# Kernel tuning notes

Hardware: AMD Instinct MI355X
Metric: run time of the kernel (lower is better)

## Reference

```python
import jax, jax.numpy as jnp
import numpy as np

B, L, D = 8, 8192, 512   # batch, seq_len (q_len == kv_len), model dim
H, K = 8, 64             # heads, head_dim
W = 128                  # chunk width == stride (non-overlapping chunks)


def setup_inputs() -> dict:
    key = jax.random.key(0)
    ks = jax.random.split(key, 6)
    s = 1.0 / np.sqrt(D)
    return {
        "inputs_q": jax.random.normal(ks[0], (B, L, D), jnp.float32),
        "inputs_kv": jax.random.normal(ks[1], (B, L, D), jnp.float32),
        "Wq": jax.random.normal(ks[2], (D, H, K), jnp.float32) * s,
        "Wk": jax.random.normal(ks[3], (D, H, K), jnp.float32) * s,
        "Wv": jax.random.normal(ks[4], (D, H, K), jnp.float32) * s,
        "Wo": jax.random.normal(ks[5], (H, K, D), jnp.float32) * s,
    }


def reference(inputs_q, inputs_kv, Wq, Wk, Wv, Wo):
    # LocalAttentionLayer with q/kv_chunk_width == stride == W and
    # always_attend_to_first_position=True. Since width == stride the chunks
    # are non-overlapping, so the per-chunk Python loop of the original is
    # equivalent to a batched reshape into [B, C, W, ...] chunks. QKV
    # projections are position-wise, so projecting the full sequence first is
    # exactly the same math as projecting each chunk.
    C = L // W  # number of chunks
    scale = 1.0 / jnp.sqrt(jnp.asarray(K, inputs_q.dtype))

    q = jnp.einsum('bld,dhk->blhk', inputs_q, Wq) * scale  # [B,L,H,K]
    k = jnp.einsum('bld,dhk->blhk', inputs_kv, Wk)
    v = jnp.einsum('bld,dhk->blhk', inputs_kv, Wv)

    qc = q.reshape(B, C, W, H, K)
    kc = k.reshape(B, C, W, H, K)
    vc = v.reshape(B, C, W, H, K)

    # Global first KV position ([CLS]) prepended to every chunk's keys/values,
    # matching `kv_cls = inputs_kv[..., 0:1, :]; concat([kv_cls, chunk])`.
    k_cls = jnp.broadcast_to(k[:, None, 0:1], (B, C, 1, H, K))
    v_cls = jnp.broadcast_to(v[:, None, 0:1], (B, C, 1, H, K))
    kc = jnp.concatenate([k_cls, kc], axis=2)  # [B,C,W+1,H,K]
    vc = jnp.concatenate([v_cls, vc], axis=2)

    scores = jnp.einsum('bcqhk,bcmhk->bchqm', qc, kc)  # [B,C,H,W,W+1]
    attn = jax.nn.softmax(scores, axis=-1)
    ctx = jnp.einsum('bchqm,bcmhk->bcqhk', attn, vc)   # [B,C,W,H,K]
    ctx = ctx.reshape(B, L, H, K)
    return jnp.einsum('blhk,hkd->bld', ctx, Wo)        # [B,L,D]
```

## Files before the change

kernel.cpp:

```cpp
#include <hip/hip_runtime.h>
#include <hip/hip_bf16.h>
#include <type_traits>

#define B_ 8
#define L_ 8192
#define D_ 512
#define H_ 8
#define KD_ 64
#define W_ 128
#define C_ 64
#define M_ (B_ * L_)
#define HK_ 512

typedef __bf16 bf16_t;
typedef __bf16 bf16x8 __attribute__((ext_vector_type(8)));
typedef float f32x4 __attribute__((ext_vector_type(4)));

#define GLOAD16(gp, lp)                                                        \
  __builtin_amdgcn_global_load_lds(                                            \
      (const __attribute__((address_space(1))) unsigned int*)(gp),             \
      (__attribute__((address_space(3))) unsigned int*)(lp), 16, 0, 0)

#define WAIT_LGKM0()                                                           \
  do {                                                                         \
    asm volatile("s_waitcnt lgkmcnt(0)" ::: "memory");                         \
    __builtin_amdgcn_sched_barrier(0);                                         \
  } while (0)

#define MFMA16(AF, BF, ACC, OFF)                                               \
  do {                                                                         \
    __builtin_amdgcn_s_setprio(1);                                             \
    _Pragma("unroll") for (int i_ = 0; i_ < 4; i_++)                           \
        _Pragma("unroll") for (int j_ = 0; j_ < 4; j_++)                       \
            ACC[i_ + OFF][j_] = __builtin_amdgcn_mfma_f32_16x16x32_bf16(       \
                AF[i_], BF[j_], ACC[i_ + OFF][j_], 0, 0, 0);                   \
    __builtin_amdgcn_s_setprio(0);                                             \
  } while (0)

__global__ void prep_weights_kernel(const float* __restrict__ Wq,
                                    const float* __restrict__ Wk,
                                    const float* __restrict__ Wv,
                                    const float* __restrict__ Wo,
                                    bf16_t* __restrict__ wt) {
  __shared__ float t[64][65];
  const int tid = threadIdx.x;
  const int mat = blockIdx.z;
  const float* src = (mat == 0) ? Wq : (mat == 1) ? Wk : (mat == 2) ? Wv : Wo;
  const float scale = (mat == 0) ? 0.125f : 1.0f;
  const int d0 = blockIdx.x * 64, n0 = blockIdx.y * 64;
  const int c = tid & 63, rb = tid >> 6;
#pragma unroll
  for (int i = 0; i < 16; i++) {
    const int r = i * 4 + rb;
    t[r][c] = src[(size_t)(d0 + r) * 512 + n0 + c];
  }
  __syncthreads();
#pragma unroll
  for (int i = 0; i < 16; i++) {
    const int n = i * 4 + rb;
    wt[((size_t)mat * 512 + n0 + n) * 512 + d0 + c] = (bf16_t)(t[c][n] * scale);
  }
}

__device__ __forceinline__ bf16x8 rdfrag(const bf16_t* region, int rowbase,
                                         int lane) {
  const int fr = lane & 15;
  const int fs = (lane >> 4) ^ ((lane >> 1) & 3);
  return *reinterpret_cast<const bf16x8*>(region + (rowbase + fr) * 32 + fs * 8);
}

__device__ __forceinline__ void rdA_raw(const float* region, int rowbase,
                                        int lane, f32x4* o) {
  const int fr = lane & 15;
  const int g = lane >> 4;
  const int row = rowbase + fr;
  const int sw = (row >> 1) & 3;
  const float* sub = region + (g >> 1) * 4096;
  const int s0 = (g & 1) << 1;
  o[0] = *reinterpret_cast<const f32x4*>(sub + row * 16 + ((s0 | 0) ^ sw) * 4);
  o[1] = *reinterpret_cast<const f32x4*>(sub + row * 16 + ((s0 | 1) ^ sw) * 4);
}

__device__ __forceinline__ bf16x8 cvtA(const f32x4* r) {
  bf16x8 o;
  o[0] = (bf16_t)r[0][0]; o[1] = (bf16_t)r[0][1];
  o[2] = (bf16_t)r[0][2]; o[3] = (bf16_t)r[0][3];
  o[4] = (bf16_t)r[1][0]; o[5] = (bf16_t)r[1][1];
  o[6] = (bf16_t)r[1][2]; o[7] = (bf16_t)r[1][3];
  return o;
}

template <int NTILE>
__global__ __launch_bounds__(512, 2)
void gemm_qkv(const float* __restrict__ A0f, const float* __restrict__ A1f,
              const bf16_t* __restrict__ BT,
              bf16_t* __restrict__ C0, bf16_t* __restrict__ C1,
              bf16_t* __restrict__ C2) {
  __shared__ __align__(16) bf16_t lds[65536];

  constexpr int NB = NTILE * 256;
  const int bid = blockIdx.x;
  const int swz = (bid & 7) * (NB / 8) + (bid >> 3);
  const int my = swz / NTILE;
  const int mx = swz - my * NTILE;
  const int m0 = my * 256;
  const int seg = mx >> 1;
  const int ncol0 = (mx & 1) * 256;
  const int nB0 = mx * 256;

  const float* const A = (seg == 0) ? A0f : A1f;
  bf16_t* const outp = (seg == 0) ? C0 : (seg == 1) ? C1 : C2;

  const int tid = threadIdx.x;
  const int lane = tid & 63;
  const int wid = tid >> 6;
  const int wmB = (wid >> 2) * 128;
  const int wnB = (wid & 3) * 64;

  const float* const Agb =
      A + ((size_t)m0 + (tid >> 2)) * 512 + (((tid & 3) ^ ((tid >> 3) & 3))) * 4;
  const int sr0 = tid >> 2;
  const int sgs = (tid & 3) ^ ((sr0 >> 1) & 3);
  const bf16_t* const Bgb = BT + ((size_t)nB0 + sr0) * 512 + sgs * 8;

  auto astage = [&](int tile, int i) {
    const int sub = i >> 1, half = i & 1;
    char* lp = (char*)lds + (tile % 3) * 32768 + sub * 16384 + half * 8192 +
               wid * 1024;
    const float* g = Agb + (size_t)half * 128 * 512 + tile * 32 + sub * 16;
    GLOAD16(g, lp);
  };
  auto bstage = [&](int tile) {
    char* lp = (char*)lds + 98304 + (tile & 1) * 16384 + wid * 1024;
    const bf16_t* g = Bgb + tile * 32;
    GLOAD16(g, lp);
    GLOAD16(g + (size_t)128 * 512, lp + 8192);
  };

  f32x4 acc[8][4] = {};
  bf16x8 b[4];

  astage(0, 0); astage(0, 1); astage(0, 2); astage(0, 3); bstage(0);
  astage(1, 0); astage(1, 1); astage(1, 2); astage(1, 3); bstage(1);
  asm volatile("s_waitcnt vmcnt(6)" ::: "memory");
  __builtin_amdgcn_s_barrier();

  for (int t = 0; t < 16; ++t) {
    const float* AR = (const float*)((char*)lds + (t % 3) * 32768);
    const bf16_t* BR = (const bf16_t*)((char*)lds + 98304 + (t & 1) * 16384);

    f32x4 ar0[4][2];
#pragma unroll
    for (int q = 0; q < 4; q++) rdA_raw(AR, wmB + q * 16, lane, ar0[q]);
#pragma unroll
    for (int q = 0; q < 4; q++) b[q] = rdfrag(BR, wnB + q * 16, lane);
    if (t < 14) { astage(t + 2, 0); astage(t + 2, 1); }
    __builtin_amdgcn_s_barrier();
    WAIT_LGKM0();
    {
      bf16x8 al[4];
#pragma unroll
      for (int q = 0; q < 4; q++) al[q] = cvtA(ar0[q]);
      MFMA16(al, b, acc, 0);
    }
    __builtin_amdgcn_s_barrier();

    f32x4 ar1[4][2];
#pragma unroll
    for (int q = 0; q < 4; q++) rdA_raw(AR, wmB + 64 + q * 16, lane, ar1[q]);
    if (t < 14) { astage(t + 2, 2); astage(t + 2, 3); bstage(t + 2); }
    __builtin_amdgcn_s_barrier();
    WAIT_LGKM0();
    {
      bf16x8 ah[4];
#pragma unroll
      for (int q = 0; q < 4; q++) ah[q] = cvtA(ar1[q]);
      MFMA16(ah, b, acc, 4);
    }
    if (t < 14) {
      asm volatile("s_waitcnt vmcnt(6)" ::: "memory");
    } else {
      asm volatile("s_waitcnt vmcnt(0)" ::: "memory");
    }
    __builtin_amdgcn_s_barrier();
  }

  const int crow = (lane >> 4) * 4;
  const int ccol = lane & 15;
#pragma unroll
  for (int i = 0; i < 8; i++) {
#pragma unroll
    for (int j = 0; j < 4; j++) {
      const int gm = m0 + wmB + i * 16 + crow;
      const int gn = ncol0 + wnB + j * 16 + ccol;
#pragma unroll
      for (int jj = 0; jj < 4; jj++)
        outp[(size_t)(gm + jj) * 512 + gn] = (bf16_t)acc[i][j][jj];
    }
  }
}

template <typename OT, int NTILE>
__global__ __launch_bounds__(512, 2)
void gemm256(const bf16_t* __restrict__ A0, const bf16_t* __restrict__ BT,
             OT* __restrict__ C0) {
  __shared__ __align__(16) bf16_t lds[65536];

  constexpr int NB = NTILE * 256;
  const int bid = blockIdx.x;
  const int swz = (bid & 7) * (NB / 8) + (bid >> 3);
  const int my = swz / NTILE;
  const int mx = swz - my * NTILE;
  const int m0 = my * 256;
  const int ncol0 = (mx & 1) * 256;
  const int nB0 = mx * 256;

  const int tid = threadIdx.x;
  const int lane = tid & 63;
  const int wid = tid >> 6;
  const int wmB = (wid >> 2) * 128;
  const int wnB = (wid & 3) * 64;

  const int sr0 = tid >> 2;
  const int sgs = (tid & 3) ^ ((sr0 >> 1) & 3);
  const bf16_t* const Agb = A0 + ((size_t)m0 + sr0) * 512 + sgs * 8;
  const bf16_t* const Bgb = BT + ((size_t)nB0 + sr0) * 512 + sgs * 8;

  auto stage = [&](int tile, int mat, int kh) {
    if (tile >= 8) return;
    bf16_t* reg = lds + ((tile & 1) * 4 + mat * 2 + kh) * 8192;
    const bf16_t* g0 = (mat == 0 ? Agb : Bgb) + tile * 64 + kh * 32;
    char* lp = (char*)reg + wid * 1024;
    GLOAD16(g0, lp);
    GLOAD16(g0 + (size_t)128 * 512, lp + 8192);
  };

  f32x4 acc[8][4] = {};
  bf16x8 a0[4], a1[4], a2[4], a3[4], b0[4], b2[4];

  stage(0, 0, 0); stage(0, 1, 0); stage(0, 0, 1); stage(0, 1, 1);
  stage(1, 1, 0); stage(1, 0, 0); stage(1, 1, 1);
  asm volatile("s_waitcnt vmcnt(6)" ::: "memory");
  __builtin_amdgcn_s_barrier();

  for (int t = 0; t < 8; ++t) {
    const int p = t & 1;
    const bf16_t* Ap0 = lds + (p * 4 + 0) * 8192;
    const bf16_t* Ap1 = lds + (p * 4 + 1) * 8192;
    const bf16_t* Bp0 = lds + (p * 4 + 2) * 8192;
    const bf16_t* Bp1 = lds + (p * 4 + 3) * 8192;

#pragma unroll
    for (int q = 0; q < 4; q++) a0[q] = rdfrag(Ap0, wmB + q * 16, lane);
#pragma unroll
    for (int q = 0; q < 4; q++) b0[q] = rdfrag(Bp0, wnB + q * 16, lane);
    stage(t + 1, 0, 1);
    __builtin_amdgcn_s_barrier();
    WAIT_LGKM0();
    if (t > 0) MFMA16(a3, b2, acc, 4);
    __builtin_amdgcn_s_barrier();

#pragma unroll
    for (int q = 0; q < 4; q++) a1[q] = rdfrag(Ap0, wmB + 64 + q * 16, lane);
    stage(t + 2, 1, 0);
    __builtin_amdgcn_s_barrier();
    WAIT_LGKM0();
    MFMA16(a0, b0, acc, 0);
    __builtin_amdgcn_s_barrier();

#pragma unroll
    for (int q = 0; q < 4; q++) a2[q] = rdfrag(Ap1, wmB + q * 16, lane);
#pragma unroll
    for (int q = 0; q < 4; q++) b2[q] = rdfrag(Bp1, wnB + q * 16, lane);
    stage(t + 2, 0, 0);
    __builtin_amdgcn_s_barrier();
    WAIT_LGKM0();
    MFMA16(a1, b0, acc, 4);
    __builtin_amdgcn_s_barrier();

#pragma unroll
    for (int q = 0; q < 4; q++) a3[q] = rdfrag(Ap1, wmB + 64 + q * 16, lane);
    stage(t + 2, 1, 1);
    __builtin_amdgcn_s_barrier();
    WAIT_LGKM0();
    MFMA16(a2, b2, acc, 0);
    if (t < 6) {
      asm volatile("s_waitcnt vmcnt(6)" ::: "memory");
    } else {
      asm volatile("s_waitcnt vmcnt(0)" ::: "memory");
    }
    __builtin_amdgcn_s_barrier();
  }

  MFMA16(a3, b2, acc, 4);

  const int crow = (lane >> 4) * 4;
  const int ccol = lane & 15;
#pragma unroll
  for (int i = 0; i < 8; i++) {
#pragma unroll
    for (int j = 0; j < 4; j++) {
      const int gm = m0 + wmB + i * 16 + crow;
      const int gn = ncol0 + wnB + j * 16 + ccol;
#pragma unroll
      for (int jj = 0; jj < 4; jj++) {
        const float vv = acc[i][j][jj];
        if constexpr (std::is_same<OT, float>::value)
          C0[(size_t)(gm + jj) * 512 + gn] = vv;
        else
          C0[(size_t)(gm + jj) * 512 + gn] = (bf16_t)vv;
      }
    }
  }
}

__global__ __launch_bounds__(256, 3)
void attn_kernel(const bf16_t* __restrict__ q, const bf16_t* __restrict__ k,
                 const bf16_t* __restrict__ v, bf16_t* __restrict__ ctx) {
  const int bid = blockIdx.x;
  const int swz = (bid & 7) * 512 + (bid >> 3);
  const int h = swz & 7;
  const int cb = swz >> 3;
  const int c = cb & 63;
  const int b = cb >> 6;

  const int tid = threadIdx.x;
  const int lane = tid & 63;
  const int w = tid >> 6;
  const int cl = lane & 15;
  const int g = lane >> 4;

  __shared__ bf16_t vT[64][136];
  __shared__ bf16_t pL[128][136];
  __shared__ float scl[128];
  __shared__ bf16_t kcls[64];
  __shared__ bf16_t vcls[64];

  const size_t headoff = (size_t)h * KD_;
  const size_t rowbase = (size_t)b * L_ + (size_t)c * W_;

  if (tid < 64) {
    kcls[tid] = k[(size_t)b * L_ * HK_ + headoff + tid];
    vcls[tid] = v[(size_t)b * L_ * HK_ + headoff + tid];
  }
  {
    const int m = tid >> 1;
    const int kd0 = (tid & 1) * 32;
    const bf16_t* vp = v + (rowbase + m) * HK_ + headoff + kd0;
#pragma unroll
    for (int i = 0; i < 4; i++) {
      bf16x8 t8 = *reinterpret_cast<const bf16x8*>(vp + i * 8);
#pragma unroll
      for (int j = 0; j < 8; j++) vT[kd0 + i * 8 + j][m] = t8[j];
    }
  }

  bf16x8 qf[2][2];
#pragma unroll
  for (int rt = 0; rt < 2; rt++)
#pragma unroll
    for (int kk = 0; kk < 2; kk++) {
      const size_t row = rowbase + w * 32 + rt * 16 + cl;
      qf[rt][kk] = *reinterpret_cast<const bf16x8*>(&q[row * HK_ + headoff + kk * 32 + g * 8]);
    }

  f32x4 sacc[2][8] = {};
#pragma unroll
  for (int ct = 0; ct < 8; ct++) {
    bf16x8 kf[2];
#pragma unroll
    for (int kk = 0; kk < 2; kk++) {
      const size_t rowm = rowbase + ct * 16 + cl;
      kf[kk] = *reinterpret_cast<const bf16x8*>(&k[rowm * HK_ + headoff + kk * 32 + g * 8]);
    }
#pragma unroll
    for (int rt = 0; rt < 2; rt++)
#pragma unroll
      for (int kk = 0; kk < 2; kk++)
        sacc[rt][ct] = __builtin_amdgcn_mfma_f32_16x16x32_bf16(qf[rt][kk], kf[kk], sacc[rt][ct], 0, 0, 0);
  }

  __syncthreads();

#pragma unroll
  for (int rt = 0; rt < 2; rt++) {
    float part = 0.f;
#pragma unroll
    for (int kk = 0; kk < 2; kk++)
#pragma unroll
      for (int j = 0; j < 8; j++)
        part += (float)qf[rt][kk][j] * (float)kcls[kk * 32 + g * 8 + j];
    part += __shfl_xor(part, 16);
    part += __shfl_xor(part, 32);
    if (g == 0) scl[w * 32 + rt * 16 + cl] = part;
  }

  float invd[2][4];
#pragma unroll
  for (int rt = 0; rt < 2; rt++) {
#pragma unroll
    for (int jj = 0; jj < 4; jj++) {
      float mx = sacc[rt][0][jj];
#pragma unroll
      for (int ct = 1; ct < 8; ct++) mx = fmaxf(mx, sacc[rt][ct][jj]);
#pragma unroll
      for (int d = 1; d < 16; d <<= 1) mx = fmaxf(mx, __shfl_xor(mx, d));
      const float sc = scl[w * 32 + rt * 16 + g * 4 + jj];
      mx = fmaxf(mx, sc);
      float sum = 0.f;
#pragma unroll
      for (int ct = 0; ct < 8; ct++) {
        const float e = __expf(sacc[rt][ct][jj] - mx);
        sacc[rt][ct][jj] = e;
        sum += e;
      }
#pragma unroll
      for (int d = 1; d < 16; d <<= 1) sum += __shfl_xor(sum, d);
      const float pc = __expf(sc - mx);
      sum += pc;
      const float inv = 1.0f / sum;
      invd[rt][jj] = inv;
      if (cl == 0) scl[w * 32 + rt * 16 + g * 4 + jj] = pc * inv;
    }
  }

#pragma unroll
  for (int rt = 0; rt < 2; rt++)
#pragma unroll
    for (int jj = 0; jj < 4; jj++) {
      const int row = w * 32 + rt * 16 + g * 4 + jj;
#pragma unroll
      for (int ct = 0; ct < 8; ct++)
        pL[row][ct * 16 + cl] = (bf16_t)(sacc[rt][ct][jj] * invd[rt][jj]);
    }
  __syncthreads();

  f32x4 cacc[2][4] = {};
#pragma unroll
  for (int kk = 0; kk < 4; kk++) {
    bf16x8 vf[4];
#pragma unroll
    for (int c2 = 0; c2 < 4; c2++)
      vf[c2] = *reinterpret_cast<const bf16x8*>(&vT[c2 * 16 + cl][kk * 32 + g * 8]);
#pragma unroll
    for (int rt = 0; rt < 2; rt++) {
      const bf16x8 pf = *reinterpret_cast<const bf16x8*>(&pL[w * 32 + rt * 16 + cl][kk * 32 + g * 8]);
#pragma unroll
      for (int c2 = 0; c2 < 4; c2++)
        cacc[rt][c2] = __builtin_amdgcn_mfma_f32_16x16x32_bf16(pf, vf[c2], cacc[rt][c2], 0, 0, 0);
    }
  }

#pragma unroll
  for (int rt = 0; rt < 2; rt++)
#pragma unroll
    for (int c2 = 0; c2 < 4; c2++)
#pragma unroll
      for (int jj = 0; jj < 4; jj++) {
        const int row = w * 32 + rt * 16 + g * 4 + jj;
        const int kd = c2 * 16 + cl;
        const float val = cacc[rt][c2][jj] + scl[row] * (float)vcls[kd];
        ctx[(rowbase + row) * HK_ + headoff + kd] = (bf16_t)val;
      }
}

extern "C" void kernel_launch(void* const* d_in, const int* in_sizes, int n_in,
                              void* d_out, int out_size, void* d_ws, size_t ws_size,
                              hipStream_t stream) {
  const float* Xq = (const float*)d_in[0];
  const float* Xkv = (const float*)d_in[1];
  const float* Wq = (const float*)d_in[2];
  const float* Wk = (const float*)d_in[3];
  const float* Wv = (const float*)d_in[4];
  const float* Wo = (const float*)d_in[5];
  float* out = (float*)d_out;

  char* ws = (char*)d_ws;
  bf16_t* wT = (bf16_t*)ws;
  size_t off = (size_t)4 * 512 * 512 * sizeof(bf16_t);
  bf16_t* qb = (bf16_t*)(ws + off); off += (size_t)M_ * HK_ * 2;
  bf16_t* kb = (bf16_t*)(ws + off); off += (size_t)M_ * HK_ * 2;
  bf16_t* vb = (bf16_t*)(ws + off); off += (size_t)M_ * HK_ * 2;
  bf16_t* ctxb = (bf16_t*)(ws + off);

  bf16_t* wTqkv = wT;
  bf16_t* wTo = wT + (size_t)3 * 512 * 512;

  prep_weights_kernel<<<dim3(8, 8, 4), 256, 0, stream>>>(Wq, Wk, Wv, Wo, wT);

  gemm_qkv<6><<<dim3(6 * (M_ / 256)), 512, 0, stream>>>(
      Xq, Xkv, wTqkv, qb, kb, vb);

  attn_kernel<<<dim3(H_ * C_ * B_), 256, 0, stream>>>(qb, kb, vb, ctxb);

  gemm256<float, 2><<<dim3(2 * (M_ / 256)), 512, 0, stream>>>(ctxb, wTo, out);
}
```

Baseline: 356.8 us.

## Write V pre-transposed per chunk/head from QKV GEMM, drop LDS transpose in attention

The QKV projection epilogue now stores V in a per-(batch, chunk, head) transposed layout [kd][row] using packed 4-element bf16 stores. The attention kernel reads V fragments directly from global memory instead of staging a transpose through LDS, which frees the vT shared array. It raises the occupancy hint from 3 to 4 blocks per SM. In exchange, V B-operand loads in the PV matmul now come from global/L2 rather than LDS, and the V stores in the GEMM epilogue are strided.

```diff
diff --git a/kernel.cpp b/kernel.cpp
--- a/kernel.cpp
+++ b/kernel.cpp
@@ -14,6 +14,7 @@
 
 typedef __bf16 bf16_t;
 typedef __bf16 bf16x8 __attribute__((ext_vector_type(8)));
+typedef __bf16 bf16x4 __attribute__((ext_vector_type(4)));
 typedef float f32x4 __attribute__((ext_vector_type(4)));
 
 #define GLOAD16(gp, lp)                                                        \
@@ -109,7 +110,6 @@
   const int nB0 = mx * 256;
 
   const float* const A = (seg == 0) ? A0f : A1f;
-  bf16_t* const outp = (seg == 0) ? C0 : (seg == 1) ? C1 : C2;
 
   const int tid = threadIdx.x;
   const int lane = tid & 63;
@@ -187,15 +187,34 @@
 
   const int crow = (lane >> 4) * 4;
   const int ccol = lane & 15;
-#pragma unroll
-  for (int i = 0; i < 8; i++) {
-#pragma unroll
-    for (int j = 0; j < 4; j++) {
-      const int gm = m0 + wmB + i * 16 + crow;
-      const int gn = ncol0 + wnB + j * 16 + ccol;
-#pragma unroll
-      for (int jj = 0; jj < 4; jj++)
-        outp[(size_t)(gm + jj) * 512 + gn] = (bf16_t)acc[i][j][jj];
+  if (seg == 2) {
+    const int cb2 = (m0 + wmB) >> 7;
+#pragma unroll
+    for (int i = 0; i < 8; i++) {
+#pragma unroll
+      for (int j = 0; j < 4; j++) {
+        const int gn = ncol0 + wnB + j * 16 + ccol;
+        const int h2 = gn >> 6, kd = gn & 63;
+        const int row = i * 16 + crow;
+        bf16x4 pk;
+#pragma unroll
+        for (int jj = 0; jj < 4; jj++) pk[jj] = (bf16_t)acc[i][j][jj];
+        *reinterpret_cast<bf16x4*>(C2 + ((size_t)(cb2 * 8 + h2)) * 8192 +
+                                   (size_t)kd * 128 + row) = pk;
+      }
+    }
+  } else {
+    bf16_t* const outp = (seg == 0) ? C0 : C1;
+#pragma unroll
+    for (int i = 0; i < 8; i++) {
+#pragma unroll
+      for (int j = 0; j < 4; j++) {
+        const int gm = m0 + wmB + i * 16 + crow;
+        const int gn = ncol0 + wnB + j * 16 + ccol;
+#pragma unroll
+        for (int jj = 0; jj < 4; jj++)
+          outp[(size_t)(gm + jj) * 512 + gn] = (bf16_t)acc[i][j][jj];
+      }
     }
   }
 }
@@ -314,9 +333,9 @@
   }
 }
 
-__global__ __launch_bounds__(256, 3)
+__global__ __launch_bounds__(256, 4)
 void attn_kernel(const bf16_t* __restrict__ q, const bf16_t* __restrict__ k,
-                 const bf16_t* __restrict__ v, bf16_t* __restrict__ ctx) {
+                 const bf16_t* __restrict__ vt, bf16_t* __restrict__ ctx) {
   const int bid = blockIdx.x;
   const int swz = (bid & 7) * 512 + (bid >> 3);
   const int h = swz & 7;
@@ -330,7 +349,6 @@
   const int cl = lane & 15;
   const int g = lane >> 4;
 
-  __shared__ bf16_t vT[64][136];
   __shared__ bf16_t pL[128][136];
   __shared__ float scl[128];
   __shared__ bf16_t kcls[64];
@@ -338,21 +356,11 @@
 
   const size_t headoff = (size_t)h * KD_;
   const size_t rowbase = (size_t)b * L_ + (size_t)c * W_;
+  const bf16_t* const vtc = vt + ((size_t)((b * 64 + c) * 8 + h)) * 8192;
 
   if (tid < 64) {
     kcls[tid] = k[(size_t)b * L_ * HK_ + headoff + tid];
-    vcls[tid] = v[(size_t)b * L_ * HK_ + headoff + tid];
-  }
-  {
-    const int m = tid >> 1;
-    const int kd0 = (tid & 1) * 32;
-    const bf16_t* vp = v + (rowbase + m) * HK_ + headoff + kd0;
-#pragma unroll
-    for (int i = 0; i < 4; i++) {
-      bf16x8 t8 = *reinterpret_cast<const bf16x8*>(vp + i * 8);
-#pragma unroll
-      for (int j = 0; j < 8; j++) vT[kd0 + i * 8 + j][m] = t8[j];
-    }
+    vcls[tid] = vt[((size_t)(b * 64 * 8 + h)) * 8192 + (size_t)tid * 128];
   }
 
   bf16x8 qf[2][2];
@@ -441,7 +449,8 @@
     bf16x8 vf[4];
 #pragma unroll
     for (int c2 = 0; c2 < 4; c2++)
-      vf[c2] = *reinterpret_cast<const bf16x8*>(&vT[c2 * 16 + cl][kk * 32 + g * 8]);
+      vf[c2] = *reinterpret_cast<const bf16x8*>(
+          &vtc[(size_t)(c2 * 16 + cl) * 128 + kk * 32 + g * 8]);
 #pragma unroll
     for (int rt = 0; rt < 2; rt++) {
       const bf16x8 pf = *reinterpret_cast<const bf16x8*>(&pL[w * 32 + rt * 16 + cl][kk * 32 + g * 8]);
@@ -480,7 +489,7 @@
   size_t off = (size_t)4 * 512 * 512 * sizeof(bf16_t);
   bf16_t* qb = (bf16_t*)(ws + off); off += (size_t)M_ * HK_ * 2;
   bf16_t* kb = (bf16_t*)(ws + off); off += (size_t)M_ * HK_ * 2;
-  bf16_t* vb = (bf16_t*)(ws + off); off += (size_t)M_ * HK_ * 2;
+  bf16_t* vtb = (bf16_t*)(ws + off); off += (size_t)M_ * HK_ * 2;
   bf16_t* ctxb = (bf16_t*)(ws + off);
 
   bf16_t* wTqkv = wT;
@@ -489,9 +498,9 @@
   prep_weights_kernel<<<dim3(8, 8, 4), 256, 0, stream>>>(Wq, Wk, Wv, Wo, wT);
 
   gemm_qkv<6><<<dim3(6 * (M_ / 256)), 512, 0, stream>>>(
-      Xq, Xkv, wTqkv, qb, kb, vb);
-
-  attn_kernel<<<dim3(H_ * C_ * B_), 256, 0, stream>>>(qb, kb, vb, ctxb);
+      Xq, Xkv, wTqkv, qb, kb, vtb);
+
+  attn_kernel<<<dim3(H_ * C_ * B_), 256, 0, stream>>>(qb, kb, vtb, ctxb);
 
   gemm256<float, 2><<<dim3(2 * (M_ / 256)), 512, 0, stream>>>(ctxb, wTo, out);
 }
```

Measured after the change: 369.2 us. 3.5% more time.
